# Optimization experiments

Measured on AMD Instinct MI355X. Metric: run time of the kernel, lower is better.

## Reference

```python
import jax, jax.numpy as jnp
import numpy as np

B, C_IN, C_OUT, H, W = 32, 256, 256, 56, 56
RATE = 0.5
K = int(C_OUT * (1.0 - RATE))  # 128 channels zeroed
BN_EPS = 1e-5


def setup_inputs() -> dict:
    key = jax.random.key(0)
    ks = jax.random.split(key, 4)
    return {
        "x": jax.random.normal(ks[0], (B, C_IN, H, W), dtype=jnp.float32),
        "conv_w": jax.random.normal(ks[1], (C_OUT, C_IN, 3, 3), dtype=jnp.float32) * 0.05,
        "gate_w": jax.random.normal(ks[2], (C_OUT, C_IN), dtype=jnp.float32) * 0.05,
        "gate_b": jnp.ones((C_OUT,), dtype=jnp.float32),
        "bn_gamma": jnp.ones((C_OUT,), dtype=jnp.float32),
        "bn_beta": jnp.zeros((C_OUT,), dtype=jnp.float32),
        "bn_mean": jnp.zeros((C_OUT,), dtype=jnp.float32),
        "bn_var": jnp.ones((C_OUT,), dtype=jnp.float32),
    }


def reference(x, conv_w, gate_w, gate_b, bn_gamma, bn_beta, bn_mean, bn_var):
    # conv2: 3x3, stride 1, padding 1, no bias  -> [B, C_OUT, H, W]
    y = jax.lax.conv_general_dilated(
        x, conv_w, window_strides=(1, 1), padding=((1, 1), (1, 1)),
        dimension_numbers=("NCHW", "OIHW", "NCHW"))
    # BatchNorm2d (eval mode: running stats)
    inv = bn_gamma / jnp.sqrt(bn_var + BN_EPS)
    y = y * inv[None, :, None, None] + (bn_beta - bn_mean * inv)[None, :, None, None]
    # use_relu=True
    y = jax.nn.relu(y)
    # gate: global abs-avg-pool -> linear -> relu   [B, C_OUT]
    s = jnp.mean(jnp.abs(x), axis=(2, 3))  # [B, C_IN]
    g = jax.nn.relu(s @ gate_w.T + gate_b)
    # zero the K smallest gate values per row (topk of -g), then renormalize
    _, idx = jax.lax.top_k(-g, K)  # indices of K smallest
    t = g.at[jnp.arange(B)[:, None], idx].set(0.0)
    t = t / jnp.sum(t, axis=1, keepdims=True) * C_OUT
    # broadcast channel mask
    return y * t[:, :, None, None]
```

## Files before the change

### kernel.cpp

```cpp
#include <hip/hip_runtime.h>
#include <hip/hip_bf16.h>
#include <cstdint>

typedef unsigned short ushort_t;
typedef unsigned int uint_t;
typedef __bf16 bf16x8 __attribute__((ext_vector_type(8)));
typedef float f32x4 __attribute__((ext_vector_type(4)));

#define B_SZ 32
#define C_IN 256
#define C_OUT 256
#define H_SZ 56
#define W_SZ 56
#define HW 3136
#define HP 58
#define WP 58
#define BN_EPS 1e-5f
#define K_ZERO 128

__device__ __forceinline__ ushort_t f2bf(float f) {
    unsigned int u = __builtin_bit_cast(unsigned int, f);
    unsigned int r = (u + 0x7fffu + ((u >> 16) & 1u)) >> 16;
    return (ushort_t)r;
}

__device__ __forceinline__ void load_lds16(const void* gptr, void* ldsptr) {
    __builtin_amdgcn_global_load_lds(
        (const __attribute__((address_space(1))) unsigned int*)(uintptr_t)gptr,
        (__attribute__((address_space(3))) unsigned int*)(uintptr_t)ldsptr,
        16, 0, 0);
}

__global__ __launch_bounds__(256) void prep_w_kernel(const float* __restrict__ w,
                                                     const float* __restrict__ gamma,
                                                     const float* __restrict__ beta,
                                                     const float* __restrict__ mean,
                                                     const float* __restrict__ var,
                                                     ushort_t* __restrict__ Wt,
                                                     float* __restrict__ bninv,
                                                     float* __restrict__ bnadd,
                                                     float* __restrict__ s) {
    int idx = blockIdx.x * 256 + threadIdx.x;
    if (idx < 9 * C_OUT * C_IN) {
        int tap = idx >> 16;
        int rem = idx & 65535;
        int co = rem >> 8, ci = rem & 255;
        Wt[idx] = f2bf(w[(size_t)(co * C_IN + ci) * 9 + tap]);
    }
    if (blockIdx.x < 32) s[idx] = 0.f;
    if (blockIdx.x == 32 && threadIdx.x < C_OUT) {
        int c = threadIdx.x;
        float inv = gamma[c] * rsqrtf(var[c] + BN_EPS);
        bninv[c] = inv;
        bnadd[c] = beta[c] - mean[c] * inv;
    }
}

__global__ __launch_bounds__(256) void prep_x_kernel(const float* __restrict__ x,
                                                     ushort_t* __restrict__ xbp,
                                                     float* __restrict__ s) {
    const int cit = blockIdx.x, h = blockIdx.y, b = blockIdx.z;
    __shared__ float tile[64][57];
    __shared__ float red2[256];
    const int t = threadIdx.x;
    const float* src = x + ((size_t)(b * C_IN + cit * 64) * H_SZ + h) * W_SZ;
    for (int i = t; i < 64 * 14; i += 256) {
        int ci = i / 14, w4 = (i - ci * 14) * 4;
        float4 v = *(const float4*)(src + (size_t)ci * HW + w4);
        tile[ci][w4] = v.x; tile[ci][w4 + 1] = v.y;
        tile[ci][w4 + 2] = v.z; tile[ci][w4 + 3] = v.w;
    }
    __syncthreads();
    {
        int ci = t & 63, wg = t >> 6;
        float a = 0.f;
#pragma unroll
        for (int j = 0; j < 14; j++) a += fabsf(tile[ci][wg * 14 + j]);
        red2[t] = a;
    }
    __syncthreads();
    if (t < 64) {
        float tot = red2[t] + red2[t + 64] + red2[t + 128] + red2[t + 192];
        atomicAdd(&s[b * C_IN + cit * 64 + t], tot * (1.0f / (float)HW));
    }
    const uint2 z2 = make_uint2(0u, 0u);
    for (int i = t; i < W_SZ * 16; i += 256) {
        int w = i >> 4, c4 = (i & 15) * 4;
        uint_t lo = (uint_t)f2bf(tile[c4][w])     | ((uint_t)f2bf(tile[c4 + 1][w]) << 16);
        uint_t hi = (uint_t)f2bf(tile[c4 + 2][w]) | ((uint_t)f2bf(tile[c4 + 3][w]) << 16);
        size_t dst = ((size_t)((b * HP + h + 1) * WP + (w + 1))) * C_IN + cit * 64 + c4;
        *(uint2*)&xbp[dst] = make_uint2(lo, hi);
    }
    if (t < 32) {
        int side = t >> 4, c4 = (t & 15) * 4;
        size_t dst = ((size_t)((b * HP + h + 1) * WP + side * 57)) * C_IN + cit * 64 + c4;
        *(uint2*)&xbp[dst] = z2;
    }
    if (h == 0 || h == 55) {
        int prow = (h == 0) ? 0 : 57;
        for (int i = t; i < 58 * 16; i += 256) {
            int w = i >> 4, c4 = (i & 15) * 4;
            size_t dst = ((size_t)((b * HP + prow) * WP + w)) * C_IN + cit * 64 + c4;
            *(uint2*)&xbp[dst] = z2;
        }
    }
}

__global__ __launch_bounds__(256) void gate_kernel(const float* __restrict__ s,
                                                   const float* __restrict__ gw,
                                                   const float* __restrict__ gb,
                                                   ushort_t* __restrict__ perm,
                                                   float* __restrict__ cscale) {
    const int b = blockIdx.x, t = threadIdx.x;
    __shared__ float sh_s[C_IN], sh_g[C_OUT], red[256];
    sh_s[t] = s[b * C_IN + t];
    __syncthreads();
    float acc = gb[t];
    const float* wr = gw + (size_t)t * C_IN;
    for (int ci = 0; ci < C_IN; ci++) acc += sh_s[ci] * wr[ci];
    float g = fmaxf(acc, 0.f);
    sh_g[t] = g;
    __syncthreads();
    int cnt = 0;
    for (int j = 0; j < C_OUT; j++) {
        float gj = sh_g[j];
        cnt += (gj < g) || (gj == g && j < t);
    }
    float tv = (cnt >= K_ZERO) ? g : 0.f;
    red[t] = tv;
    __syncthreads();
    for (int off = 128; off > 0; off >>= 1) {
        if (t < off) red[t] += red[t + off];
        __syncthreads();
    }
    if (cnt >= K_ZERO) {
        int pos = cnt - K_ZERO;
        perm[b * C_OUT + pos] = (ushort_t)t;
        cscale[b * K_ZERO + pos] = tv * ((float)C_OUT / red[0]);
    } else {
        perm[b * C_OUT + K_ZERO + cnt] = (ushort_t)t;
    }
}

__global__ __launch_bounds__(256, 3) void conv_kernel(const ushort_t* __restrict__ xbp,
                                                      const ushort_t* __restrict__ Wt,
                                                      const float* __restrict__ bninv,
                                                      const float* __restrict__ bnadd,
                                                      const ushort_t* __restrict__ perm,
                                                      const float* __restrict__ cscale,
                                                      float* __restrict__ out) {
    __shared__ __align__(16) ushort_t As[128 * 64];
    __shared__ __align__(16) ushort_t Bs[128 * 64];
    const int t = threadIdx.x;
    const int bxr = blockIdx.x;
    const int L = (bxr & 7) * 100 + (bxr >> 3);
    const int b = L / 25;
    const int tile = L - b * 25;
    const int lane = t & 63;
    const int wv = t >> 6;
    const int waveM = wv >> 1, waveN = wv & 1;

    const int srow = t >> 3;
    const int gxor8 = ((t & 7) ^ (srow & 7)) * 8;
    int arow[4], wrow[4];
#pragma unroll
    for (int i = 0; i < 4; i++) {
        int pl = tile * 128 + i * 32 + srow;
        pl = pl < HW ? pl : HW - 1;
        int hh = pl / W_SZ, ww = pl - hh * W_SZ;
        arow[i] = ((b * HP + hh + 1) * WP + (ww + 1)) * C_IN + gxor8;
        int co = perm[b * C_OUT + i * 32 + srow];
        wrow[i] = co * C_IN + gxor8;
    }
    ushort_t* ldsA = As + t * 8;
    ushort_t* ldsB = Bs + t * 8;

    int aoff[2][4], boff[2][4];
#pragma unroll
    for (int ks = 0; ks < 2; ks++) {
        int c = (lane >> 4) + ks * 4;
#pragma unroll
        for (int mt = 0; mt < 4; mt++) {
            int ra = waveM * 64 + mt * 16 + (lane & 15);
            aoff[ks][mt] = (ra * 8 + (c ^ (ra & 7))) * 16;
            int rb = waveN * 64 + mt * 16 + (lane & 15);
            boff[ks][mt] = (rb * 8 + (c ^ (rb & 7))) * 16;
        }
    }

    f32x4 acc[4][4];
#pragma unroll
    for (int i = 0; i < 4; i++)
#pragma unroll
        for (int j = 0; j < 4; j++) acc[i][j] = (f32x4){0.f, 0.f, 0.f, 0.f};

    const char* Ab = (const char*)As;
    const char* Bb = (const char*)Bs;

    for (int cq = 0; cq < 4; cq++) {
        const int ci0 = cq * 64;
        for (int tap = 0; tap < 9; tap++) {
            const int doff = ((tap / 3 - 1) * WP + (tap % 3 - 1)) * C_IN;
            const int woff = tap * (C_OUT * C_IN);
#pragma unroll
            for (int i = 0; i < 4; i++) {
                load_lds16(xbp + arow[i] + doff + ci0, ldsA + i * 2048);
                load_lds16(Wt + wrow[i] + woff + ci0, ldsB + i * 2048);
            }
            __syncthreads();
#pragma unroll
            for (int ks = 0; ks < 2; ks++) {
                bf16x8 af[4], bf[4];
#pragma unroll
                for (int mt = 0; mt < 4; mt++) af[mt] = *(const bf16x8*)(Ab + aoff[ks][mt]);
#pragma unroll
                for (int nt = 0; nt < 4; nt++) bf[nt] = *(const bf16x8*)(Bb + boff[ks][nt]);
#pragma unroll
                for (int mt = 0; mt < 4; mt++)
#pragma unroll
                    for (int nt = 0; nt < 4; nt++)
                        acc[mt][nt] = __builtin_amdgcn_mfma_f32_16x16x32_bf16(
                            af[mt], bf[nt], acc[mt][nt], 0, 0, 0);
            }
            __syncthreads();
        }
    }

    int coK[4], coD[4];
    float invK[4], addK[4], tscK[4];
#pragma unroll
    for (int nt = 0; nt < 4; nt++) {
        int j = waveN * 64 + nt * 16 + (lane & 15);
        coK[nt] = perm[b * C_OUT + j];
        coD[nt] = perm[b * C_OUT + K_ZERO + j];
        invK[nt] = bninv[coK[nt]];
        addK[nt] = bnadd[coK[nt]];
        tscK[nt] = cscale[b * K_ZERO + j];
    }
    const float4 z4 = make_float4(0.f, 0.f, 0.f, 0.f);
#pragma unroll
    for (int mt = 0; mt < 4; mt++) {
        int pl0 = tile * 128 + waveM * 64 + mt * 16 + (lane >> 4) * 4;
        if (pl0 < HW) {
#pragma unroll
            for (int nt = 0; nt < 4; nt++) {
                float inv = invK[nt], add = addK[nt], tsc = tscK[nt];
                float4 o;
                o.x = fmaxf(acc[mt][nt][0] * inv + add, 0.f) * tsc;
                o.y = fmaxf(acc[mt][nt][1] * inv + add, 0.f) * tsc;
                o.z = fmaxf(acc[mt][nt][2] * inv + add, 0.f) * tsc;
                o.w = fmaxf(acc[mt][nt][3] * inv + add, 0.f) * tsc;
                *(float4*)(out + (size_t)(b * C_OUT + coK[nt]) * HW + pl0) = o;
                *(float4*)(out + (size_t)(b * C_OUT + coD[nt]) * HW + pl0) = z4;
            }
        }
    }
}

extern "C" void kernel_launch(void* const* d_in, const int* in_sizes, int n_in,
                              void* d_out, int out_size, void* d_ws, size_t ws_size,
                              hipStream_t stream) {
    const float* x      = (const float*)d_in[0];
    const float* conv_w = (const float*)d_in[1];
    const float* gate_w = (const float*)d_in[2];
    const float* gate_b = (const float*)d_in[3];
    const float* bn_g   = (const float*)d_in[4];
    const float* bn_b   = (const float*)d_in[5];
    const float* bn_m   = (const float*)d_in[6];
    const float* bn_v   = (const float*)d_in[7];
    float* out = (float*)d_out;

    char* ws = (char*)d_ws;
    float*    s      = (float*)(ws + 0);
    ushort_t* perm   = (ushort_t*)(ws + 32768);
    float*    cscale = (float*)(ws + 49152);
    float*    bninv  = (float*)(ws + 65536);
    float*    bnadd  = (float*)(ws + 66560);
    ushort_t* Wt     = (ushort_t*)(ws + 67584);
    ushort_t* xbp    = (ushort_t*)(ws + 1247232);

    prep_w_kernel<<<2304, 256, 0, stream>>>(conv_w, bn_g, bn_b, bn_m, bn_v, Wt, bninv, bnadd, s);
    prep_x_kernel<<<dim3(4, 56, 32), 256, 0, stream>>>(x, xbp, s);
    gate_kernel<<<32, 256, 0, stream>>>(s, gate_w, gate_b, perm, cscale);
    conv_kernel<<<dim3(25 * 32), 256, 0, stream>>>(xbp, Wt, bninv, bnadd, perm, cscale, out);
}
```

Before: 323.2 us.

## Load padded input window once per channel chunk and reuse across 3x3 taps

Instead of reloading a 128-pixel A tile from global memory for each of the nine taps, each block loads a 256-row window of the padded input, covering the tile plus halo, into LDS once per 64-channel chunk. Each tap then reads the shifted rows from that window. Only the weight tiles are still loaded per tap. Block-to-(batch, tile) mapping is also changed, which alters L2 locality. The cost is a doubled A buffer in LDS, which may reduce occupancy. The window is a fixed 256 rows, and correctness depends on it covering the 128-pixel tile plus the one-row halo on each side.

```diff
diff --git a/kernel.cpp b/kernel.cpp
--- a/kernel.cpp
+++ b/kernel.cpp
@@ -15,6 +15,7 @@
 #define HW 3136
 #define HP 58
 #define WP 58
+#define PPAD 3364
 #define BN_EPS 1e-5f
 #define K_ZERO 128
 
@@ -149,43 +150,56 @@
                                                       const ushort_t* __restrict__ perm,
                                                       const float* __restrict__ cscale,
                                                       float* __restrict__ out) {
-    __shared__ __align__(16) ushort_t As[128 * 64];
+    __shared__ __align__(16) ushort_t Aw[256 * 64];
     __shared__ __align__(16) ushort_t Bs[128 * 64];
     const int t = threadIdx.x;
     const int bxr = blockIdx.x;
-    const int L = (bxr & 7) * 100 + (bxr >> 3);
-    const int b = L / 25;
-    const int tile = L - b * 25;
+    const int idx = bxr >> 3;
+    const int b = (bxr & 7) * 4 + (idx & 3);
+    const int tile = idx >> 2;
     const int lane = t & 63;
     const int wv = t >> 6;
     const int waveM = wv >> 1, waveN = wv & 1;
 
+    const int p0 = tile * 128;
+    const int h0 = p0 / W_SZ, w0 = p0 - h0 * W_SZ;
+    const int pp0 = (h0 + 1) * WP + (w0 + 1);
+
     const int srow = t >> 3;
     const int gxor8 = ((t & 7) ^ (srow & 7)) * 8;
-    int arow[4], wrow[4];
+    int awin[8], wrowB[4];
+#pragma unroll
+    for (int i = 0; i < 8; i++) {
+        int wrow_g = pp0 - 59 + i * 32 + srow;
+        wrow_g = wrow_g > (PPAD - 1) ? (PPAD - 1) : wrow_g;
+        awin[i] = (b * PPAD + wrow_g) * C_IN + gxor8;
+    }
 #pragma unroll
     for (int i = 0; i < 4; i++) {
-        int pl = tile * 128 + i * 32 + srow;
+        int co = perm[b * C_OUT + i * 32 + srow];
+        wrowB[i] = co * C_IN + gxor8;
+    }
+    ushort_t* ldsA = Aw + t * 8;
+    ushort_t* ldsB = Bs + t * 8;
+
+    int boff[2][4];
+#pragma unroll
+    for (int ks = 0; ks < 2; ks++) {
+        int c = (lane >> 4) + ks * 4;
+#pragma unroll
+        for (int nt = 0; nt < 4; nt++) {
+            int rb = waveN * 64 + nt * 16 + (lane & 15);
+            boff[ks][nt] = (rb * 8 + (c ^ (rb & 7))) * 16;
+        }
+    }
+
+    int wrb[4];
+#pragma unroll
+    for (int mt = 0; mt < 4; mt++) {
+        int pl = p0 + waveM * 64 + mt * 16 + (lane & 15);
         pl = pl < HW ? pl : HW - 1;
         int hh = pl / W_SZ, ww = pl - hh * W_SZ;
-        arow[i] = ((b * HP + hh + 1) * WP + (ww + 1)) * C_IN + gxor8;
-        int co = perm[b * C_OUT + i * 32 + srow];
-        wrow[i] = co * C_IN + gxor8;
-    }
-    ushort_t* ldsA = As + t * 8;
-    ushort_t* ldsB = Bs + t * 8;
-
-    int aoff[2][4], boff[2][4];
-#pragma unroll
-    for (int ks = 0; ks < 2; ks++) {
-        int c = (lane >> 4) + ks * 4;
-#pragma unroll
-        for (int mt = 0; mt < 4; mt++) {
-            int ra = waveM * 64 + mt * 16 + (lane & 15);
-            aoff[ks][mt] = (ra * 8 + (c ^ (ra & 7))) * 16;
-            int rb = waveN * 64 + mt * 16 + (lane & 15);
-            boff[ks][mt] = (rb * 8 + (c ^ (rb & 7))) * 16;
-        }
+        wrb[mt] = (hh + 1) * WP + (ww + 1) - pp0 + 59;
     }
 
     f32x4 acc[4][4];
@@ -194,27 +208,32 @@
 #pragma unroll
         for (int j = 0; j < 4; j++) acc[i][j] = (f32x4){0.f, 0.f, 0.f, 0.f};
 
-    const char* Ab = (const char*)As;
-    const char* Bb = (const char*)Bs;
+    const char* Abc = (const char*)Aw;
+    const char* Bbc = (const char*)Bs;
 
     for (int cq = 0; cq < 4; cq++) {
         const int ci0 = cq * 64;
+#pragma unroll
+        for (int i = 0; i < 8; i++)
+            load_lds16(xbp + awin[i] + ci0, ldsA + i * 2048);
         for (int tap = 0; tap < 9; tap++) {
-            const int doff = ((tap / 3 - 1) * WP + (tap % 3 - 1)) * C_IN;
+            const int dtap = (tap / 3 - 1) * WP + (tap % 3 - 1);
             const int woff = tap * (C_OUT * C_IN);
 #pragma unroll
-            for (int i = 0; i < 4; i++) {
-                load_lds16(xbp + arow[i] + doff + ci0, ldsA + i * 2048);
-                load_lds16(Wt + wrow[i] + woff + ci0, ldsB + i * 2048);
-            }
+            for (int i = 0; i < 4; i++)
+                load_lds16(Wt + wrowB[i] + woff + ci0, ldsB + i * 2048);
             __syncthreads();
 #pragma unroll
             for (int ks = 0; ks < 2; ks++) {
                 bf16x8 af[4], bf[4];
-#pragma unroll
-                for (int mt = 0; mt < 4; mt++) af[mt] = *(const bf16x8*)(Ab + aoff[ks][mt]);
-#pragma unroll
-                for (int nt = 0; nt < 4; nt++) bf[nt] = *(const bf16x8*)(Bb + boff[ks][nt]);
+                const int c = (lane >> 4) + ks * 4;
+#pragma unroll
+                for (int mt = 0; mt < 4; mt++) {
+                    int wr = wrb[mt] + dtap;
+                    af[mt] = *(const bf16x8*)(Abc + wr * 128 + ((c ^ (wr & 7)) << 4));
+                }
+#pragma unroll
+                for (int nt = 0; nt < 4; nt++) bf[nt] = *(const bf16x8*)(Bbc + boff[ks][nt]);
 #pragma unroll
                 for (int mt = 0; mt < 4; mt++)
 #pragma unroll
@@ -240,7 +259,7 @@
     const float4 z4 = make_float4(0.f, 0.f, 0.f, 0.f);
 #pragma unroll
     for (int mt = 0; mt < 4; mt++) {
-        int pl0 = tile * 128 + waveM * 64 + mt * 16 + (lane >> 4) * 4;
+        int pl0 = p0 + waveM * 64 + mt * 16 + (lane >> 4) * 4;
         if (pl0 < HW) {
 #pragma unroll
             for (int nt = 0; nt < 4; nt++) {
```

After: 350.7 us. 8.5% more time.
